# Kernel tuning notes

Hardware: AMD Instinct MI355X
Metric: run time of the kernel (lower is better)

## Reference

```python
import jax, jax.numpy as jnp
import numpy as np

E, TOPK, H, I = 8, 2, 2048, 5632
T = 4096


def setup_inputs() -> dict:
    key = jax.random.key(0)
    k1, k2, k3, k4 = jax.random.split(key, 4)
    hidden_states = jax.random.normal(k1, (T, H), dtype=jnp.float32)
    gate_w = jax.random.normal(k2, (E, H), dtype=jnp.float32) * (1.0 / np.sqrt(H))
    # fused gate+up projection: [E, 2*I, H]
    w13 = jax.random.normal(k3, (E, 2 * I, H), dtype=jnp.float32) * (1.0 / np.sqrt(H))
    # down projection: [E, H, I]
    w2 = jax.random.normal(k4, (E, H, I), dtype=jnp.float32) * (1.0 / np.sqrt(I))
    return {"hidden_states": hidden_states, "gate_w": gate_w, "w13": w13, "w2": w2, "top_k": TOPK}


def reference(hidden_states, gate_w, w13, w2, top_k):
    num_experts = gate_w.shape[0]
    inter = w2.shape[2]
    # router: fp32 gate logits -> softmax -> top-k -> renormalize (FusedMoE renormalize=True)
    logits = hidden_states.astype(jnp.float32) @ gate_w.T          # [T, E]
    probs = jax.nn.softmax(logits, axis=-1)
    vals, idx = jax.lax.top_k(probs, top_k)                        # [T, k]
    vals = vals / jnp.sum(vals, axis=-1, keepdims=True)
    # dense routing weight matrix [T, E] (zero outside top-k)
    dense_w = jnp.sum(jax.nn.one_hot(idx, num_experts, dtype=vals.dtype) * vals[..., None], axis=1)

    def body(acc, inputs):
        w13_e, w2_e, we = inputs                                   # [2I,H], [H,I], [T]
        gu = hidden_states @ w13_e.T                               # [T, 2I]
        g, u = gu[:, :inter], gu[:, inter:]
        h = jax.nn.silu(g) * u                                     # SwiGLU
        y = h @ w2_e.T                                             # [T, H]
        return acc + we[:, None] * y, None

    acc0 = jnp.zeros_like(hidden_states)
    out, _ = jax.lax.scan(body, acc0, (w13, w2, dense_w.T))
    return out
```

## Files before the change

### kernel.cpp

```cpp
#include <hip/hip_runtime.h>

#define T_TOK 4096
#define H_DIM 2048
#define I_DIM 5632
#define NE 8

typedef _Float16 f16;
typedef _Float16 f16x8 __attribute__((ext_vector_type(8)));
typedef _Float16 f16x4 __attribute__((ext_vector_type(4)));
typedef float f32x4 __attribute__((ext_vector_type(4)));

#define OFF_META   0
#define OFF_BTOK   256
#define OFF_BW     (256 + 32768)
#define OFF_RE     (256 + 2 * 32768)
#define OFF_RW     (256 + 3 * 32768)
#define OFF_HSB    (256 + 4 * 32768)
#define OFF_HB     (OFF_HSB + (size_t)T_TOK * H_DIM * 2)

__device__ __forceinline__ int swzk(int r, int bir) {
    return (bir & 15) | ((((bir >> 4) ^ r) & 7) << 4);
}

__device__ __forceinline__ f16x4 cvt4(float4 v) {
    f16x4 t; t[0] = (f16)v.x; t[1] = (f16)v.y; t[2] = (f16)v.z; t[3] = (f16)v.w; return t;
}

__global__ void cvt_hs_kernel(const float* __restrict__ hs, f16* __restrict__ hsb) {
    size_t i = ((size_t)blockIdx.x * 256 + threadIdx.x) * 8;
    float4 a = *(const float4*)(hs + i);
    float4 b = *(const float4*)(hs + i + 4);
    f16x8 v;
    v[0] = (f16)a.x; v[1] = (f16)a.y; v[2] = (f16)a.z; v[3] = (f16)a.w;
    v[4] = (f16)b.x; v[5] = (f16)b.y; v[6] = (f16)b.z; v[7] = (f16)b.w;
    *(f16x8*)(hsb + i) = v;
}

__global__ void gate_kernel(const float* __restrict__ hs, const float* __restrict__ gw,
                            int* __restrict__ re, float* __restrict__ rw,
                            int* __restrict__ counts) {
    int lane = threadIdx.x & 63;
    int t = blockIdx.x * 4 + (threadIdx.x >> 6);
    float acc[NE];
#pragma unroll
    for (int e = 0; e < NE; ++e) acc[e] = 0.f;
    const float* x = hs + (size_t)t * H_DIM;
    for (int i = lane; i < H_DIM; i += 64) {
        float xv = x[i];
#pragma unroll
        for (int e = 0; e < NE; ++e) acc[e] += xv * gw[e * H_DIM + i];
    }
#pragma unroll
    for (int e = 0; e < NE; ++e)
        for (int off = 32; off > 0; off >>= 1) acc[e] += __shfl_xor(acc[e], off);
    if (lane == 0) {
        int i1 = 0; float l1 = acc[0];
#pragma unroll
        for (int e = 1; e < NE; ++e) if (acc[e] > l1) { l1 = acc[e]; i1 = e; }
        int i2 = -1; float l2 = -1e30f;
#pragma unroll
        for (int e = 0; e < NE; ++e) if (e != i1 && acc[e] > l2) { l2 = acc[e]; i2 = e; }
        float aa = __expf(l2 - l1);
        float s = 1.f / (1.f + aa);
        re[t * 2] = i1; re[t * 2 + 1] = i2;
        rw[t * 2] = s;  rw[t * 2 + 1] = aa * s;
        atomicAdd(&counts[i1], 1);
        atomicAdd(&counts[i2], 1);
    }
}

__global__ void scan_kernel(int* __restrict__ meta) {
    if (threadIdx.x == 0) {
        int s = 0;
        for (int e = 0; e < NE; ++e) { meta[8 + e] = s; meta[16 + e] = s; s += meta[e]; }
    }
}

__global__ void place_kernel(const int* __restrict__ re, const float* __restrict__ rw,
                             int* __restrict__ cursor, int* __restrict__ btok,
                             float* __restrict__ bwv) {
    int t = blockIdx.x * 256 + threadIdx.x;
    if (t >= T_TOK) return;
#pragma unroll
    for (int s = 0; s < 2; ++s) {
        int e = re[t * 2 + s];
        int p = atomicAdd(&cursor[e], 1);
        btok[p] = t;
        bwv[p] = rw[t * 2 + s];
    }
}

__device__ __forceinline__ void decode_panel(int id, int npx, int e_arg,
                                             int& e, int& bx, int& by) {
    int sg  = id >> 8;
    int rem = id & 255;
    by = rem >> 3;
    int P = sg * 8 + (rem & 7);
    if (e_arg >= 0) { e = e_arg; bx = P; }
    else            { e = P / npx; bx = P % npx; }
}

__global__ __launch_bounds__(512) void gemm1_kernel(
    const float* __restrict__ w13, const f16* __restrict__ hsb, f16* __restrict__ hb,
    const int* __restrict__ counts, const int* __restrict__ offs,
    const int* __restrict__ btok, int e_arg, int global_h)
{
    int e, bx, by;
    decode_panel(blockIdx.x, 88, e_arg, e, bx, by);
    const int n_e = counts[e];
    if (by * 128 >= n_e) return;
    const int boff = offs[e];
    const float* We = w13 + (size_t)e * (2 * I_DIM) * H_DIM;

    const int tid = threadIdx.x;
    const int lane = tid & 63;
    const int wid = tid >> 6;
    const int wm = wid >> 1, wn = wid & 1;

    __shared__ f16 As[128 * 64];
    __shared__ f16 Bg[64 * 64];
    __shared__ f16 Bu[64 * 64];
    char* AsB = (char*)As; char* BgB = (char*)Bg; char* BuB = (char*)Bu;

    const f16* gA[2];
    int awadr[2];
#pragma unroll
    for (int i = 0; i < 2; ++i) {
        int c = i * 512 + tid;
        int r = c >> 3;
        int s = c & 7;
        int idx = by * 128 + r;
        idx = idx < n_e ? idx : n_e - 1;
        int tok = btok[boff + idx];
        gA[i] = hsb + (size_t)tok * H_DIM + s * 8;
        awadr[i] = r * 128 + swzk(r, s * 16);
    }
    const float* gBg[2]; const float* gBu[2];
    int bwadr[2];
#pragma unroll
    for (int j = 0; j < 2; ++j) {
        int c = j * 512 + tid;
        int r = c >> 4;
        int k4 = c & 15;
        gBg[j] = We + (size_t)(bx * 64 + r) * H_DIM + k4 * 4;
        gBu[j] = We + (size_t)(I_DIM + bx * 64 + r) * H_DIM + k4 * 4;
        bwadr[j] = r * 128 + swzk(r, k4 * 8);
    }

    f32x4 accg[2][2], accu[2][2];
#pragma unroll
    for (int m = 0; m < 2; ++m)
#pragma unroll
        for (int n = 0; n < 2; ++n) { accg[m][n] = (f32x4)0.f; accu[m][n] = (f32x4)0.f; }

    const int NT = H_DIM / 64;

    f16x8 aR[2]; float4 gR[2], uR[2];
#pragma unroll
    for (int i = 0; i < 2; ++i) {
        aR[i] = *(const f16x8*)(gA[i]);
        gR[i] = *(const float4*)(gBg[i]);
        uR[i] = *(const float4*)(gBu[i]);
    }

#pragma unroll 1
    for (int kt = 0; kt < NT; ++kt) {
        __syncthreads();
#pragma unroll
        for (int i = 0; i < 2; ++i) {
            *(f16x8*)(AsB + awadr[i]) = aR[i];
            *(f16x4*)(BgB + bwadr[i]) = cvt4(gR[i]);
            *(f16x4*)(BuB + bwadr[i]) = cvt4(uR[i]);
        }
        __syncthreads();
        if (kt + 1 < NT) {
            int k0 = (kt + 1) * 64;
#pragma unroll
            for (int i = 0; i < 2; ++i) {
                aR[i] = *(const f16x8*)(gA[i] + k0);
                gR[i] = *(const float4*)(gBg[i] + k0);
                uR[i] = *(const float4*)(gBu[i] + k0);
            }
        }
#pragma unroll
        for (int kh = 0; kh < 2; ++kh) {
            f16x8 a[2], bg[2], bu[2];
            const int kb = kh * 64 + (lane >> 4) * 16;
#pragma unroll
            for (int m = 0; m < 2; ++m) {
                int r = wm * 32 + m * 16 + (lane & 15);
                a[m] = *(const f16x8*)(AsB + r * 128 + swzk(r, kb));
            }
#pragma unroll
            for (int n = 0; n < 2; ++n) {
                int r = wn * 32 + n * 16 + (lane & 15);
                bg[n] = *(const f16x8*)(BgB + r * 128 + swzk(r, kb));
                bu[n] = *(const f16x8*)(BuB + r * 128 + swzk(r, kb));
            }
#pragma unroll
            for (int m = 0; m < 2; ++m)
#pragma unroll
                for (int n = 0; n < 2; ++n) {
                    accg[m][n] = __builtin_amdgcn_mfma_f32_16x16x32_f16(a[m], bg[n], accg[m][n], 0, 0, 0);
                    accu[m][n] = __builtin_amdgcn_mfma_f32_16x16x32_f16(a[m], bu[n], accu[m][n], 0, 0, 0);
                }
        }
    }

    const int hbase = (global_h ? boff : 0) + by * 128;
#pragma unroll
    for (int m = 0; m < 2; ++m) {
        int rl0 = wm * 32 + m * 16 + ((lane >> 4) << 2);
#pragma unroll
        for (int r = 0; r < 4; ++r) {
            int rl = rl0 + r;
            if (by * 128 + rl < n_e) {
#pragma unroll
                for (int n = 0; n < 2; ++n) {
                    float g = accg[m][n][r];
                    float u = accu[m][n][r];
                    float h = g / (1.f + __expf(-g)) * u;
                    hb[(size_t)(hbase + rl) * I_DIM + bx * 64 + wn * 32 + n * 16 + (lane & 15)] = (f16)h;
                }
            }
        }
    }
}

__global__ __launch_bounds__(512) void gemm2_kernel(
    const float* __restrict__ w2, const f16* __restrict__ hb, float* __restrict__ out,
    const int* __restrict__ counts, const int* __restrict__ offs,
    const int* __restrict__ btok, const float* __restrict__ bwv, int e_arg, int global_h)
{
    int e, bx, by;
    decode_panel(blockIdx.x, 16, e_arg, e, bx, by);
    const int n_e = counts[e];
    if (by * 128 >= n_e) return;
    const int boff = offs[e];
    const float* We = w2 + (size_t)e * H_DIM * I_DIM;

    const int tid = threadIdx.x;
    const int lane = tid & 63;
    const int wid = tid >> 6;
    const int wm = wid >> 1, wn = wid & 1;

    __shared__ f16 As[128 * 64];
    __shared__ f16 Bs[128 * 64];
    char* AsB = (char*)As; char* BsB = (char*)Bs;

    const int hbase = (global_h ? boff : 0) + by * 128;
    const f16* gA[2];
    int awadr[2];
#pragma unroll
    for (int i = 0; i < 2; ++i) {
        int c = i * 512 + tid;
        int r = c >> 3;
        int s = c & 7;
        gA[i] = hb + (size_t)(hbase + r) * I_DIM + s * 8;
        awadr[i] = r * 128 + swzk(r, s * 16);
    }
    const float* gB[4];
    int bwadr[4];
#pragma unroll
    for (int j = 0; j < 4; ++j) {
        int c = j * 512 + tid;
        int r = c >> 4;
        int k4 = c & 15;
        gB[j] = We + (size_t)(bx * 128 + r) * I_DIM + k4 * 4;
        bwadr[j] = r * 128 + swzk(r, k4 * 8);
    }

    f32x4 acc[2][4];
#pragma unroll
    for (int m = 0; m < 2; ++m)
#pragma unroll
        for (int n = 0; n < 4; ++n) acc[m][n] = (f32x4)0.f;

    const int NT = I_DIM / 64;

    f16x8 aR[2]; float4 bR[4];
#pragma unroll
    for (int i = 0; i < 2; ++i) aR[i] = *(const f16x8*)(gA[i]);
#pragma unroll
    for (int j = 0; j < 4; ++j) bR[j] = *(const float4*)(gB[j]);

#pragma unroll 1
    for (int kt = 0; kt < NT; ++kt) {
        __syncthreads();
#pragma unroll
        for (int i = 0; i < 2; ++i) *(f16x8*)(AsB + awadr[i]) = aR[i];
#pragma unroll
        for (int j = 0; j < 4; ++j) *(f16x4*)(BsB + bwadr[j]) = cvt4(bR[j]);
        __syncthreads();
        if (kt + 1 < NT) {
            int k0 = (kt + 1) * 64;
#pragma unroll
            for (int i = 0; i < 2; ++i) aR[i] = *(const f16x8*)(gA[i] + k0);
#pragma unroll
            for (int j = 0; j < 4; ++j) bR[j] = *(const float4*)(gB[j] + k0);
        }
#pragma unroll
        for (int kh = 0; kh < 2; ++kh) {
            f16x8 a[2], b[4];
            const int kb = kh * 64 + (lane >> 4) * 16;
#pragma unroll
            for (int m = 0; m < 2; ++m) {
                int r = wm * 32 + m * 16 + (lane & 15);
                a[m] = *(const f16x8*)(AsB + r * 128 + swzk(r, kb));
            }
#pragma unroll
            for (int n = 0; n < 4; ++n) {
                int r = wn * 64 + n * 16 + (lane & 15);
                b[n] = *(const f16x8*)(BsB + r * 128 + swzk(r, kb));
            }
#pragma unroll
            for (int m = 0; m < 2; ++m)
#pragma unroll
                for (int n = 0; n < 4; ++n)
                    acc[m][n] = __builtin_amdgcn_mfma_f32_16x16x32_f16(a[m], b[n], acc[m][n], 0, 0, 0);
        }
    }

#pragma unroll
    for (int m = 0; m < 2; ++m) {
        int rl0 = wm * 32 + m * 16 + ((lane >> 4) << 2);
#pragma unroll
        for (int r = 0; r < 4; ++r) {
            int rl = rl0 + r;
            if (by * 128 + rl < n_e) {
                int p = boff + by * 128 + rl;
                int tok = btok[p];
                float w = bwv[p];
#pragma unroll
                for (int n = 0; n < 4; ++n)
                    atomicAdd(&out[(size_t)tok * H_DIM + bx * 128 + wn * 64 + n * 16 + (lane & 15)],
                              w * acc[m][n][r]);
            }
        }
    }
}

extern "C" void kernel_launch(void* const* d_in, const int* in_sizes, int n_in,
                              void* d_out, int out_size, void* d_ws, size_t ws_size,
                              hipStream_t stream) {
    const float* hs  = (const float*)d_in[0];
    const float* gw  = (const float*)d_in[1];
    const float* w13 = (const float*)d_in[2];
    const float* w2  = (const float*)d_in[3];
    float* out = (float*)d_out;

    char* ws = (char*)d_ws;
    int*   meta = (int*)(ws + OFF_META);
    int*   btok = (int*)(ws + OFF_BTOK);
    float* bwv  = (float*)(ws + OFF_BW);
    int*   re   = (int*)(ws + OFF_RE);
    float* rw   = (float*)(ws + OFF_RW);
    f16*   hsb  = (f16*)(ws + OFF_HSB);
    f16*   hb   = (f16*)(ws + OFF_HB);

    hipMemsetAsync(d_out, 0, (size_t)T_TOK * H_DIM * 4, stream);
    hipMemsetAsync(meta, 0, 256, stream);

    cvt_hs_kernel<<<(T_TOK * H_DIM) / (256 * 8), 256, 0, stream>>>(hs, hsb);
    gate_kernel<<<T_TOK / 4, 256, 0, stream>>>(hs, gw, re, rw, meta);
    scan_kernel<<<1, 64, 0, stream>>>(meta);
    place_kernel<<<T_TOK / 256, 256, 0, stream>>>(re, rw, meta + 16, btok, bwv);

    size_t need_allpairs = OFF_HB + (size_t)(2 * T_TOK + 128) * I_DIM * 2;
    if (ws_size >= need_allpairs) {
        gemm1_kernel<<<704 * 32, 512, 0, stream>>>(w13, hsb, hb, meta, meta + 8, btok, -1, 1);
        gemm2_kernel<<<128 * 32, 512, 0, stream>>>(w2, hb, out, meta, meta + 8, btok, bwv, -1, 1);
    } else {
        for (int e = 0; e < NE; ++e) {
            gemm1_kernel<<<88 * 32, 512, 0, stream>>>(w13, hsb, hb, meta, meta + 8, btok, e, 0);
            gemm2_kernel<<<16 * 32, 512, 0, stream>>>(w2, hb, out, meta, meta + 8, btok, bwv, e, 0);
        }
    }
}
```

Baseline: 1.152 ms.

## Double-buffer shared memory tiles in both MoE GEMM kernels

Both GEMM kernels switch from a single shared-memory tile with two barriers per K step to ping-pong buffers with one barrier per step. Global loads for the next tile are issued before the MFMA work on the current buffer and written to the other buffer afterward. This overlaps LDS stores and global latency with compute and halves barrier count. LDS usage doubles (up to 64 KB for gemm2), which may lower occupancy.

New measurement: 1.330 ms. 1.15x slower.

```diff
diff --git a/kernel.cpp b/kernel.cpp
--- a/kernel.cpp
+++ b/kernel.cpp
@@ -117,10 +117,9 @@
     const int wid = tid >> 6;
     const int wm = wid >> 1, wn = wid & 1;
 
-    __shared__ f16 As[128 * 64];
-    __shared__ f16 Bg[64 * 64];
-    __shared__ f16 Bu[64 * 64];
-    char* AsB = (char*)As; char* BgB = (char*)Bg; char* BuB = (char*)Bu;
+    __shared__ f16 As0[128 * 64], As1[128 * 64];
+    __shared__ f16 Bg0[64 * 64],  Bg1[64 * 64];
+    __shared__ f16 Bu0[64 * 64],  Bu1[64 * 64];
 
     const f16* gA[2];
     int awadr[2];
@@ -155,57 +154,72 @@
 
     const int NT = H_DIM / 64;
 
-    f16x8 aR[2]; float4 gR[2], uR[2];
-#pragma unroll
-    for (int i = 0; i < 2; ++i) {
-        aR[i] = *(const f16x8*)(gA[i]);
-        gR[i] = *(const float4*)(gBg[i]);
-        uR[i] = *(const float4*)(gBu[i]);
-    }
-
-#pragma unroll 1
-    for (int kt = 0; kt < NT; ++kt) {
-        __syncthreads();
-#pragma unroll
-        for (int i = 0; i < 2; ++i) {
-            *(f16x8*)(AsB + awadr[i]) = aR[i];
-            *(f16x4*)(BgB + bwadr[i]) = cvt4(gR[i]);
-            *(f16x4*)(BuB + bwadr[i]) = cvt4(uR[i]);
+    {
+        f16x8 aP[2]; float4 gP[2], uP[2];
+#pragma unroll
+        for (int i = 0; i < 2; ++i) aP[i] = *(const f16x8*)(gA[i]);
+#pragma unroll
+        for (int j = 0; j < 2; ++j) { gP[j] = *(const float4*)gBg[j]; uP[j] = *(const float4*)gBu[j]; }
+#pragma unroll
+        for (int i = 0; i < 2; ++i) *(f16x8*)((char*)As0 + awadr[i]) = aP[i];
+#pragma unroll
+        for (int j = 0; j < 2; ++j) {
+            *(f16x4*)((char*)Bg0 + bwadr[j]) = cvt4(gP[j]);
+            *(f16x4*)((char*)Bu0 + bwadr[j]) = cvt4(uP[j]);
         }
         __syncthreads();
-        if (kt + 1 < NT) {
-            int k0 = (kt + 1) * 64;
-#pragma unroll
-            for (int i = 0; i < 2; ++i) {
-                aR[i] = *(const f16x8*)(gA[i] + k0);
-                gR[i] = *(const float4*)(gBg[i] + k0);
-                uR[i] = *(const float4*)(gBu[i] + k0);
-            }
-        }
-#pragma unroll
-        for (int kh = 0; kh < 2; ++kh) {
-            f16x8 a[2], bg[2], bu[2];
-            const int kb = kh * 64 + (lane >> 4) * 16;
-#pragma unroll
-            for (int m = 0; m < 2; ++m) {
-                int r = wm * 32 + m * 16 + (lane & 15);
-                a[m] = *(const f16x8*)(AsB + r * 128 + swzk(r, kb));
-            }
-#pragma unroll
-            for (int n = 0; n < 2; ++n) {
-                int r = wn * 32 + n * 16 + (lane & 15);
-                bg[n] = *(const f16x8*)(BgB + r * 128 + swzk(r, kb));
-                bu[n] = *(const f16x8*)(BuB + r * 128 + swzk(r, kb));
-            }
-#pragma unroll
-            for (int m = 0; m < 2; ++m)
-#pragma unroll
-                for (int n = 0; n < 2; ++n) {
-                    accg[m][n] = __builtin_amdgcn_mfma_f32_16x16x32_f16(a[m], bg[n], accg[m][n], 0, 0, 0);
-                    accu[m][n] = __builtin_amdgcn_mfma_f32_16x16x32_f16(a[m], bu[n], accu[m][n], 0, 0, 0);
-                }
-        }
-    }
+    }
+
+#define G1_TILE(AsR, BgR, BuR, AsW, BgW, BuW, t)                                    \
+    {                                                                               \
+        const int kn = (((t) + 1 < NT) ? (t) + 1 : NT - 1) * 64;                    \
+        f16x8 aN[2]; float4 gN[2], uN[2];                                           \
+        _Pragma("unroll")                                                           \
+        for (int i = 0; i < 2; ++i) aN[i] = *(const f16x8*)(gA[i] + kn);            \
+        _Pragma("unroll")                                                           \
+        for (int j = 0; j < 2; ++j) {                                               \
+            gN[j] = *(const float4*)(gBg[j] + kn);                                  \
+            uN[j] = *(const float4*)(gBu[j] + kn);                                  \
+        }                                                                           \
+        _Pragma("unroll")                                                           \
+        for (int kh = 0; kh < 2; ++kh) {                                            \
+            f16x8 a[2], bg[2], bu[2];                                               \
+            const int kb = kh * 64 + (lane >> 4) * 16;                              \
+            _Pragma("unroll")                                                       \
+            for (int m = 0; m < 2; ++m) {                                           \
+                int r = wm * 32 + m * 16 + (lane & 15);                             \
+                a[m] = *(const f16x8*)((const char*)AsR + r * 128 + swzk(r, kb));   \
+            }                                                                       \
+            _Pragma("unroll")                                                       \
+            for (int n = 0; n < 2; ++n) {                                           \
+                int r = wn * 32 + n * 16 + (lane & 15);                             \
+                bg[n] = *(const f16x8*)((const char*)BgR + r * 128 + swzk(r, kb));  \
+                bu[n] = *(const f16x8*)((const char*)BuR + r * 128 + swzk(r, kb));  \
+            }                                                                       \
+            _Pragma("unroll")                                                       \
+            for (int m = 0; m < 2; ++m)                                             \
+                _Pragma("unroll")                                                   \
+                for (int n = 0; n < 2; ++n) {                                       \
+                    accg[m][n] = __builtin_amdgcn_mfma_f32_16x16x32_f16(a[m], bg[n], accg[m][n], 0, 0, 0); \
+                    accu[m][n] = __builtin_amdgcn_mfma_f32_16x16x32_f16(a[m], bu[n], accu[m][n], 0, 0, 0); \
+                }                                                                   \
+        }                                                                           \
+        _Pragma("unroll")                                                           \
+        for (int i = 0; i < 2; ++i) *(f16x8*)((char*)AsW + awadr[i]) = aN[i];       \
+        _Pragma("unroll")                                                           \
+        for (int j = 0; j < 2; ++j) {                                               \
+            *(f16x4*)((char*)BgW + bwadr[j]) = cvt4(gN[j]);                         \
+            *(f16x4*)((char*)BuW + bwadr[j]) = cvt4(uN[j]);                         \
+        }                                                                           \
+        __syncthreads();                                                            \
+    }
+
+#pragma unroll 1
+    for (int kt = 0; kt < NT; kt += 2) {
+        G1_TILE(As0, Bg0, Bu0, As1, Bg1, Bu1, kt);
+        G1_TILE(As1, Bg1, Bu1, As0, Bg0, Bu0, kt + 1);
+    }
+#undef G1_TILE
 
     const int hbase = (global_h ? boff : 0) + by * 128;
 #pragma unroll
@@ -244,9 +258,8 @@
     const int wid = tid >> 6;
     const int wm = wid >> 1, wn = wid & 1;
 
-    __shared__ f16 As[128 * 64];
-    __shared__ f16 Bs[128 * 64];
-    char* AsB = (char*)As; char* BsB = (char*)Bs;
+    __shared__ f16 As0[128 * 64], As1[128 * 64];
+    __shared__ f16 Bs0[128 * 64], Bs1[128 * 64];
 
     const int hbase = (global_h ? boff : 0) + by * 128;
     const f16* gA[2];
@@ -278,48 +291,60 @@
 
     const int NT = I_DIM / 64;
 
-    f16x8 aR[2]; float4 bR[4];
-#pragma unroll
-    for (int i = 0; i < 2; ++i) aR[i] = *(const f16x8*)(gA[i]);
-#pragma unroll
-    for (int j = 0; j < 4; ++j) bR[j] = *(const float4*)(gB[j]);
+    {
+        f16x8 aP[2]; float4 bP[4];
+#pragma unroll
+        for (int i = 0; i < 2; ++i) aP[i] = *(const f16x8*)(gA[i]);
+#pragma unroll
+        for (int j = 0; j < 4; ++j) bP[j] = *(const float4*)gB[j];
+#pragma unroll
+        for (int i = 0; i < 2; ++i) *(f16x8*)((char*)As0 + awadr[i]) = aP[i];
+#pragma unroll
+        for (int j = 0; j < 4; ++j) *(f16x4*)((char*)Bs0 + bwadr[j]) = cvt4(bP[j]);
+        __syncthreads();
+    }
+
+#define G2_TILE(AsR, BsR, AsW, BsW, t)                                              \
+    {                                                                               \
+        const int kn = (((t) + 1 < NT) ? (t) + 1 : NT - 1) * 64;                    \
+        f16x8 aN[2]; float4 bN[4];                                                  \
+        _Pragma("unroll")                                                           \
+        for (int i = 0; i < 2; ++i) aN[i] = *(const f16x8*)(gA[i] + kn);            \
+        _Pragma("unroll")                                                           \
+        for (int j = 0; j < 4; ++j) bN[j] = *(const float4*)(gB[j] + kn);           \
+        _Pragma("unroll")                                                           \
+        for (int kh = 0; kh < 2; ++kh) {                                            \
+            f16x8 a[2], b[4];                                                       \
+            const int kb = kh * 64 + (lane >> 4) * 16;                              \
+            _Pragma("unroll")                                                       \
+            for (int m = 0; m < 2; ++m) {                                           \
+                int r = wm * 32 + m * 16 + (lane & 15);                             \
+                a[m] = *(const f16x8*)((const char*)AsR + r * 128 + swzk(r, kb));   \
+            }                                                                       \
+            _Pragma("unroll")                                                       \
+            for (int n = 0; n < 4; ++n) {                                           \
+                int r = wn * 64 + n * 16 + (lane & 15);                             \
+                b[n] = *(const f16x8*)((const char*)BsR + r * 128 + swzk(r, kb));   \
+            }                                                                       \
+            _Pragma("unroll")                                                       \
+            for (int m = 0; m < 2; ++m)                                             \
+                _Pragma("unroll")                                                   \
+                for (int n = 0; n < 4; ++n)                                         \
+                    acc[m][n] = __builtin_amdgcn_mfma_f32_16x16x32_f16(a[m], b[n], acc[m][n], 0, 0, 0); \
+        }                                                                           \
+        _Pragma("unroll")                                                           \
+        for (int i = 0; i < 2; ++i) *(f16x8*)((char*)AsW + awadr[i]) = aN[i];       \
+        _Pragma("unroll")                                                           \
+        for (int j = 0; j < 4; ++j) *(f16x4*)((char*)BsW + bwadr[j]) = cvt4(bN[j]); \
+        __syncthreads();                                                            \
+    }
 
 #pragma unroll 1
-    for (int kt = 0; kt < NT; ++kt) {
-        __syncthreads();
-#pragma unroll
-        for (int i = 0; i < 2; ++i) *(f16x8*)(AsB + awadr[i]) = aR[i];
-#pragma unroll
-        for (int j = 0; j < 4; ++j) *(f16x4*)(BsB + bwadr[j]) = cvt4(bR[j]);
-        __syncthreads();
-        if (kt + 1 < NT) {
-            int k0 = (kt + 1) * 64;
-#pragma unroll
-            for (int i = 0; i < 2; ++i) aR[i] = *(const f16x8*)(gA[i] + k0);
-#pragma unroll
-            for (int j = 0; j < 4; ++j) bR[j] = *(const float4*)(gB[j] + k0);
-        }
-#pragma unroll
-        for (int kh = 0; kh < 2; ++kh) {
-            f16x8 a[2], b[4];
-            const int kb = kh * 64 + (lane >> 4) * 16;
-#pragma unroll
-            for (int m = 0; m < 2; ++m) {
-                int r = wm * 32 + m * 16 + (lane & 15);
-                a[m] = *(const f16x8*)(AsB + r * 128 + swzk(r, kb));
-            }
-#pragma unroll
-            for (int n = 0; n < 4; ++n) {
-                int r = wn * 64 + n * 16 + (lane & 15);
-                b[n] = *(const f16x8*)(BsB + r * 128 + swzk(r, kb));
-            }
-#pragma unroll
-            for (int m = 0; m < 2; ++m)
-#pragma unroll
-                for (int n = 0; n < 4; ++n)
-                    acc[m][n] = __builtin_amdgcn_mfma_f32_16x16x32_f16(a[m], b[n], acc[m][n], 0, 0, 0);
-        }
-    }
+    for (int kt = 0; kt < NT; kt += 2) {
+        G2_TILE(As0, Bs0, As1, Bs1, kt);
+        G2_TILE(As1, Bs1, As0, Bs0, kt + 1);
+    }
+#undef G2_TILE
 
 #pragma unroll
     for (int m = 0; m < 2; ++m) {
```

## Double-buffer MoE GEMMs with direct global-to-LDS loads and larger tiles

Applied to the files above, without the earlier changes.

Both expert GEMM kernels move to 128x256 tiles with 8 waves arranged 2x4. LDS is double-buffered, and activations load straight into LDS through global_load_lds using a pre-swizzled source. The fp32 weight loads are split into two halves that are converted and staged while MFMAs run, with raw waitcnt/barrier control and setprio around the MFMA bursts. Launch grids shrink to match. The aim is to hide global latency and raise MFMA reuse per loaded byte, at the cost of more LDS and registers (launch_bounds 512,2) and fragile hand-managed waitcnts.

Result: slower. 1.648 ms (+43.1%).

```diff
diff --git a/kernel.cpp b/kernel.cpp
--- a/kernel.cpp
+++ b/kernel.cpp
@@ -18,12 +18,23 @@
 #define OFF_HSB    (256 + 4 * 32768)
 #define OFF_HB     (OFF_HSB + (size_t)T_TOK * H_DIM * 2)
 
+typedef const __attribute__((address_space(1))) unsigned int guint;
+typedef __attribute__((address_space(3))) unsigned int luint;
+
+#define WAITVM8()   asm volatile("s_waitcnt vmcnt(8)" ::: "memory")
+#define WAITVM0()   asm volatile("s_waitcnt vmcnt(0)" ::: "memory")
+#define LGKM0_SB()  do { asm volatile("s_waitcnt lgkmcnt(0)" ::: "memory"); __builtin_amdgcn_sched_barrier(0); } while (0)
+
 __device__ __forceinline__ int swzk(int r, int bir) {
     return (bir & 15) | ((((bir >> 4) ^ r) & 7) << 4);
 }
 
 __device__ __forceinline__ f16x4 cvt4(float4 v) {
     f16x4 t; t[0] = (f16)v.x; t[1] = (f16)v.y; t[2] = (f16)v.z; t[3] = (f16)v.w; return t;
+}
+
+__device__ __forceinline__ f16x8 ldsr(const char* base, int r, int kb) {
+    return *(const f16x8*)(base + r * 128 + swzk(r, kb));
 }
 
 __global__ void cvt_hs_kernel(const float* __restrict__ hs, f16* __restrict__ hsb) {
@@ -92,238 +103,326 @@
 
 __device__ __forceinline__ void decode_panel(int id, int npx, int e_arg,
                                              int& e, int& bx, int& by) {
+    if (e_arg >= 0) { e = e_arg; bx = id >> 5; by = id & 31; return; }
     int sg  = id >> 8;
     int rem = id & 255;
     by = rem >> 3;
     int P = sg * 8 + (rem & 7);
-    if (e_arg >= 0) { e = e_arg; bx = P; }
-    else            { e = P / npx; bx = P % npx; }
-}
-
-__global__ __launch_bounds__(512) void gemm1_kernel(
+    e = P / npx; bx = P % npx;
+}
+
+__global__ __launch_bounds__(512, 2) void gemm1_kernel(
     const float* __restrict__ w13, const f16* __restrict__ hsb, f16* __restrict__ hb,
     const int* __restrict__ counts, const int* __restrict__ offs,
     const int* __restrict__ btok, int e_arg, int global_h)
 {
     int e, bx, by;
-    decode_panel(blockIdx.x, 88, e_arg, e, bx, by);
+    decode_panel(blockIdx.x, 44, e_arg, e, bx, by);
     const int n_e = counts[e];
     if (by * 128 >= n_e) return;
     const int boff = offs[e];
     const float* We = w13 + (size_t)e * (2 * I_DIM) * H_DIM;
 
-    const int tid = threadIdx.x;
+    const int tid  = threadIdx.x;
     const int lane = tid & 63;
-    const int wid = tid >> 6;
-    const int wm = wid >> 1, wn = wid & 1;
-
-    __shared__ f16 As[128 * 64];
-    __shared__ f16 Bg[64 * 64];
-    __shared__ f16 Bu[64 * 64];
-    char* AsB = (char*)As; char* BgB = (char*)Bg; char* BuB = (char*)Bu;
+    const int wid  = tid >> 6;
+    const int wm   = wid >> 2;
+    const int wn   = wid & 3;
+    const int l15  = lane & 15;
+    const int klo  = (lane >> 4) * 16;
+
+    __shared__ f16 As[2][128 * 64];
+    __shared__ f16 Bs[2][256 * 64];
+    char* AsB = (char*)As; char* BsB = (char*)Bs;
 
     const f16* gA[2];
-    int awadr[2];
+    int adst[2];
 #pragma unroll
     for (int i = 0; i < 2; ++i) {
         int c = i * 512 + tid;
         int r = c >> 3;
-        int s = c & 7;
         int idx = by * 128 + r;
         idx = idx < n_e ? idx : n_e - 1;
         int tok = btok[boff + idx];
-        gA[i] = hsb + (size_t)tok * H_DIM + s * 8;
-        awadr[i] = r * 128 + swzk(r, s * 16);
-    }
-    const float* gBg[2]; const float* gBu[2];
-    int bwadr[2];
-#pragma unroll
-    for (int j = 0; j < 2; ++j) {
+        gA[i] = hsb + (size_t)tok * H_DIM + ((c & 7) ^ (r & 7)) * 8;
+        adst[i] = c * 16;
+    }
+    const float* gB[8];
+    int bwadr[8];
+#pragma unroll
+    for (int j = 0; j < 8; ++j) {
         int c = j * 512 + tid;
-        int r = c >> 4;
+        int row = c >> 4;
         int k4 = c & 15;
-        gBg[j] = We + (size_t)(bx * 64 + r) * H_DIM + k4 * 4;
-        gBu[j] = We + (size_t)(I_DIM + bx * 64 + r) * H_DIM + k4 * 4;
-        bwadr[j] = r * 128 + swzk(r, k4 * 8);
-    }
-
-    f32x4 accg[2][2], accu[2][2];
-#pragma unroll
-    for (int m = 0; m < 2; ++m)
-#pragma unroll
-        for (int n = 0; n < 2; ++n) { accg[m][n] = (f32x4)0.f; accu[m][n] = (f32x4)0.f; }
+        int wrow = (row < 128) ? (bx * 128 + row) : (I_DIM + bx * 128 + (row - 128));
+        gB[j] = We + (size_t)wrow * H_DIM + k4 * 4;
+        bwadr[j] = row * 128 + swzk(row, k4 * 8);
+    }
+
+    f32x4 ag[4][2], au[4][2];
+#pragma unroll
+    for (int m = 0; m < 4; ++m)
+#pragma unroll
+        for (int n = 0; n < 2; ++n) { ag[m][n] = (f32x4)0.f; au[m][n] = (f32x4)0.f; }
 
     const int NT = H_DIM / 64;
 
-    f16x8 aR[2]; float4 gR[2], uR[2];
-#pragma unroll
-    for (int i = 0; i < 2; ++i) {
-        aR[i] = *(const f16x8*)(gA[i]);
-        gR[i] = *(const float4*)(gBg[i]);
-        uR[i] = *(const float4*)(gBu[i]);
-    }
+    float4 bX[4], bY[4];
+#pragma unroll
+    for (int i = 0; i < 2; ++i)
+        __builtin_amdgcn_global_load_lds((guint*)gA[i], (luint*)(AsB + adst[i]), 16, 0, 0);
+#pragma unroll
+    for (int j = 0; j < 4; ++j) bX[j] = *(const float4*)gB[j];
+#pragma unroll
+    for (int j = 0; j < 4; ++j) bY[j] = *(const float4*)gB[j + 4];
+#pragma unroll
+    for (int j = 0; j < 4; ++j) *(f16x4*)(BsB + bwadr[j])     = cvt4(bX[j]);
+#pragma unroll
+    for (int j = 0; j < 4; ++j) *(f16x4*)(BsB + bwadr[j + 4]) = cvt4(bY[j]);
+#pragma unroll
+    for (int j = 0; j < 4; ++j) bX[j] = *(const float4*)(gB[j] + 64);
+#pragma unroll
+    for (int j = 0; j < 4; ++j) bY[j] = *(const float4*)(gB[j + 4] + 64);
+    asm volatile("s_waitcnt lgkmcnt(0)" ::: "memory");
+    __builtin_amdgcn_s_barrier();
 
 #pragma unroll 1
     for (int kt = 0; kt < NT; ++kt) {
-        __syncthreads();
-#pragma unroll
-        for (int i = 0; i < 2; ++i) {
-            *(f16x8*)(AsB + awadr[i]) = aR[i];
-            *(f16x4*)(BgB + bwadr[i]) = cvt4(gR[i]);
-            *(f16x4*)(BuB + bwadr[i]) = cvt4(uR[i]);
-        }
-        __syncthreads();
-        if (kt + 1 < NT) {
-            int k0 = (kt + 1) * 64;
-#pragma unroll
-            for (int i = 0; i < 2; ++i) {
-                aR[i] = *(const f16x8*)(gA[i] + k0);
-                gR[i] = *(const float4*)(gBg[i] + k0);
-                uR[i] = *(const float4*)(gBu[i] + k0);
-            }
-        }
-#pragma unroll
-        for (int kh = 0; kh < 2; ++kh) {
-            f16x8 a[2], bg[2], bu[2];
-            const int kb = kh * 64 + (lane >> 4) * 16;
-#pragma unroll
-            for (int m = 0; m < 2; ++m) {
-                int r = wm * 32 + m * 16 + (lane & 15);
-                a[m] = *(const f16x8*)(AsB + r * 128 + swzk(r, kb));
-            }
-#pragma unroll
-            for (int n = 0; n < 2; ++n) {
-                int r = wn * 32 + n * 16 + (lane & 15);
-                bg[n] = *(const f16x8*)(BgB + r * 128 + swzk(r, kb));
-                bu[n] = *(const f16x8*)(BuB + r * 128 + swzk(r, kb));
-            }
-#pragma unroll
-            for (int m = 0; m < 2; ++m)
-#pragma unroll
-                for (int n = 0; n < 2; ++n) {
-                    accg[m][n] = __builtin_amdgcn_mfma_f32_16x16x32_f16(a[m], bg[n], accg[m][n], 0, 0, 0);
-                    accu[m][n] = __builtin_amdgcn_mfma_f32_16x16x32_f16(a[m], bu[n], accu[m][n], 0, 0, 0);
-                }
-        }
-    }
+        const int cur = kt & 1;
+        const int kA = ((kt + 1 < NT) ? kt + 1 : NT - 1) * 64;
+        const int kB = ((kt + 2 < NT) ? kt + 2 : NT - 1) * 64;
+        const char* Ab = AsB + cur * 16384;
+        const char* Bb = BsB + cur * 32768;
+        char* Aw = AsB + (cur ^ 1) * 16384;
+        char* Bw = BsB + (cur ^ 1) * 32768;
+        {
+#pragma unroll
+            for (int i = 0; i < 2; ++i)
+                __builtin_amdgcn_global_load_lds((guint*)(gA[i] + kA), (luint*)(Aw + adst[i]), 16, 0, 0);
+            f16x8 af[2][4], bf[2][2];
+#pragma unroll
+            for (int kh = 0; kh < 2; ++kh) {
+                const int kb = kh * 64 + klo;
+#pragma unroll
+                for (int mf = 0; mf < 4; ++mf) af[kh][mf] = ldsr(Ab, wm * 64 + mf * 16 + l15, kb);
+#pragma unroll
+                for (int nf = 0; nf < 2; ++nf) bf[kh][nf] = ldsr(Bb, wn * 32 + nf * 16 + l15, kb);
+            }
+#pragma unroll
+            for (int j = 0; j < 4; ++j) *(f16x4*)(Bw + bwadr[j]) = cvt4(bX[j]);
+            __builtin_amdgcn_s_barrier();
+            LGKM0_SB();
+            __builtin_amdgcn_s_setprio(1);
+#pragma unroll
+            for (int kh = 0; kh < 2; ++kh)
+#pragma unroll
+                for (int mf = 0; mf < 4; ++mf)
+#pragma unroll
+                    for (int nf = 0; nf < 2; ++nf)
+                        ag[mf][nf] = __builtin_amdgcn_mfma_f32_16x16x32_f16(af[kh][mf], bf[kh][nf], ag[mf][nf], 0, 0, 0);
+            __builtin_amdgcn_s_setprio(0);
+            __builtin_amdgcn_s_barrier();
+        }
+        {
+#pragma unroll
+            for (int j = 0; j < 4; ++j) bX[j] = *(const float4*)(gB[j] + kB);
+            f16x8 af[2][4], bf[2][2];
+#pragma unroll
+            for (int kh = 0; kh < 2; ++kh) {
+                const int kb = kh * 64 + klo;
+#pragma unroll
+                for (int mf = 0; mf < 4; ++mf) af[kh][mf] = ldsr(Ab, wm * 64 + mf * 16 + l15, kb);
+#pragma unroll
+                for (int nf = 0; nf < 2; ++nf) bf[kh][nf] = ldsr(Bb, 128 + wn * 32 + nf * 16 + l15, kb);
+            }
+#pragma unroll
+            for (int j = 0; j < 4; ++j) *(f16x4*)(Bw + bwadr[j + 4]) = cvt4(bY[j]);
+#pragma unroll
+            for (int j = 0; j < 4; ++j) bY[j] = *(const float4*)(gB[j + 4] + kB);
+            __builtin_amdgcn_s_barrier();
+            LGKM0_SB();
+            __builtin_amdgcn_s_setprio(1);
+#pragma unroll
+            for (int kh = 0; kh < 2; ++kh)
+#pragma unroll
+                for (int mf = 0; mf < 4; ++mf)
+#pragma unroll
+                    for (int nf = 0; nf < 2; ++nf)
+                        au[mf][nf] = __builtin_amdgcn_mfma_f32_16x16x32_f16(af[kh][mf], bf[kh][nf], au[mf][nf], 0, 0, 0);
+            __builtin_amdgcn_s_setprio(0);
+            WAITVM8();
+            __builtin_amdgcn_s_barrier();
+        }
+    }
+    WAITVM0();
 
     const int hbase = (global_h ? boff : 0) + by * 128;
 #pragma unroll
-    for (int m = 0; m < 2; ++m) {
-        int rl0 = wm * 32 + m * 16 + ((lane >> 4) << 2);
+    for (int mf = 0; mf < 4; ++mf) {
+        int rl0 = wm * 64 + mf * 16 + ((lane >> 4) << 2);
 #pragma unroll
         for (int r = 0; r < 4; ++r) {
             int rl = rl0 + r;
             if (by * 128 + rl < n_e) {
 #pragma unroll
-                for (int n = 0; n < 2; ++n) {
-                    float g = accg[m][n][r];
-                    float u = accu[m][n][r];
+                for (int nf = 0; nf < 2; ++nf) {
+                    float g = ag[mf][nf][r];
+                    float u = au[mf][nf][r];
                     float h = g / (1.f + __expf(-g)) * u;
-                    hb[(size_t)(hbase + rl) * I_DIM + bx * 64 + wn * 32 + n * 16 + (lane & 15)] = (f16)h;
+                    hb[(size_t)(hbase + rl) * I_DIM + bx * 128 + wn * 32 + nf * 16 + l15] = (f16)h;
                 }
             }
         }
     }
 }
 
-__global__ __launch_bounds__(512) void gemm2_kernel(
+__global__ __launch_bounds__(512, 2) void gemm2_kernel(
     const float* __restrict__ w2, const f16* __restrict__ hb, float* __restrict__ out,
     const int* __restrict__ counts, const int* __restrict__ offs,
     const int* __restrict__ btok, const float* __restrict__ bwv, int e_arg, int global_h)
 {
     int e, bx, by;
-    decode_panel(blockIdx.x, 16, e_arg, e, bx, by);
+    decode_panel(blockIdx.x, 8, e_arg, e, bx, by);
     const int n_e = counts[e];
     if (by * 128 >= n_e) return;
     const int boff = offs[e];
     const float* We = w2 + (size_t)e * H_DIM * I_DIM;
 
-    const int tid = threadIdx.x;
+    const int tid  = threadIdx.x;
     const int lane = tid & 63;
-    const int wid = tid >> 6;
-    const int wm = wid >> 1, wn = wid & 1;
-
-    __shared__ f16 As[128 * 64];
-    __shared__ f16 Bs[128 * 64];
+    const int wid  = tid >> 6;
+    const int wm   = wid >> 2;
+    const int wn   = wid & 3;
+    const int l15  = lane & 15;
+    const int klo  = (lane >> 4) * 16;
+
+    __shared__ f16 As[2][128 * 64];
+    __shared__ f16 Bs[2][256 * 64];
     char* AsB = (char*)As; char* BsB = (char*)Bs;
 
-    const int hbase = (global_h ? boff : 0) + by * 128;
+    const int hb0 = global_h ? boff : 0;
     const f16* gA[2];
-    int awadr[2];
+    int adst[2];
 #pragma unroll
     for (int i = 0; i < 2; ++i) {
         int c = i * 512 + tid;
         int r = c >> 3;
-        int s = c & 7;
-        gA[i] = hb + (size_t)(hbase + r) * I_DIM + s * 8;
-        awadr[i] = r * 128 + swzk(r, s * 16);
-    }
-    const float* gB[4];
-    int bwadr[4];
-#pragma unroll
-    for (int j = 0; j < 4; ++j) {
+        int idx = by * 128 + r;
+        idx = idx < n_e ? idx : n_e - 1;
+        gA[i] = hb + (size_t)(hb0 + idx) * I_DIM + ((c & 7) ^ (r & 7)) * 8;
+        adst[i] = c * 16;
+    }
+    const float* gB[8];
+    int bwadr[8];
+#pragma unroll
+    for (int j = 0; j < 8; ++j) {
         int c = j * 512 + tid;
-        int r = c >> 4;
+        int row = c >> 4;
         int k4 = c & 15;
-        gB[j] = We + (size_t)(bx * 128 + r) * I_DIM + k4 * 4;
-        bwadr[j] = r * 128 + swzk(r, k4 * 8);
-    }
-
-    f32x4 acc[2][4];
-#pragma unroll
-    for (int m = 0; m < 2; ++m)
+        gB[j] = We + (size_t)(bx * 256 + row) * I_DIM + k4 * 4;
+        bwadr[j] = row * 128 + swzk(row, k4 * 8);
+    }
+
+    f32x4 acc[4][4];
+#pragma unroll
+    for (int m = 0; m < 4; ++m)
 #pragma unroll
         for (int n = 0; n < 4; ++n) acc[m][n] = (f32x4)0.f;
 
     const int NT = I_DIM / 64;
 
-    f16x8 aR[2]; float4 bR[4];
-#pragma unroll
-    for (int i = 0; i < 2; ++i) aR[i] = *(const f16x8*)(gA[i]);
-#pragma unroll
-    for (int j = 0; j < 4; ++j) bR[j] = *(const float4*)(gB[j]);
+    float4 bX[4], bY[4];
+#pragma unroll
+    for (int i = 0; i < 2; ++i)
+        __builtin_amdgcn_global_load_lds((guint*)gA[i], (luint*)(AsB + adst[i]), 16, 0, 0);
+#pragma unroll
+    for (int j = 0; j < 4; ++j) bX[j] = *(const float4*)gB[j];
+#pragma unroll
+    for (int j = 0; j < 4; ++j) bY[j] = *(const float4*)gB[j + 4];
+#pragma unroll
+    for (int j = 0; j < 4; ++j) *(f16x4*)(BsB + bwadr[j])     = cvt4(bX[j]);
+#pragma unroll
+    for (int j = 0; j < 4; ++j) *(f16x4*)(BsB + bwadr[j + 4]) = cvt4(bY[j]);
+#pragma unroll
+    for (int j = 0; j < 4; ++j) bX[j] = *(const float4*)(gB[j] + 64);
+#pragma unroll
+    for (int j = 0; j < 4; ++j) bY[j] = *(const float4*)(gB[j + 4] + 64);
+    asm volatile("s_waitcnt lgkmcnt(0)" ::: "memory");
+    __builtin_amdgcn_s_barrier();
 
 #pragma unroll 1
     for (int kt = 0; kt < NT; ++kt) {
-        __syncthreads();
-#pragma unroll
-        for (int i = 0; i < 2; ++i) *(f16x8*)(AsB + awadr[i]) = aR[i];
-#pragma unroll
-        for (int j = 0; j < 4; ++j) *(f16x4*)(BsB + bwadr[j]) = cvt4(bR[j]);
-        __syncthreads();
-        if (kt + 1 < NT) {
-            int k0 = (kt + 1) * 64;
-#pragma unroll
-            for (int i = 0; i < 2; ++i) aR[i] = *(const f16x8*)(gA[i] + k0);
-#pragma unroll
-            for (int j = 0; j < 4; ++j) bR[j] = *(const float4*)(gB[j] + k0);
-        }
-#pragma unroll
-        for (int kh = 0; kh < 2; ++kh) {
-            f16x8 a[2], b[4];
-            const int kb = kh * 64 + (lane >> 4) * 16;
-#pragma unroll
-            for (int m = 0; m < 2; ++m) {
-                int r = wm * 32 + m * 16 + (lane & 15);
-                a[m] = *(const f16x8*)(AsB + r * 128 + swzk(r, kb));
-            }
-#pragma unroll
-            for (int n = 0; n < 4; ++n) {
-                int r = wn * 64 + n * 16 + (lane & 15);
-                b[n] = *(const f16x8*)(BsB + r * 128 + swzk(r, kb));
-            }
-#pragma unroll
-            for (int m = 0; m < 2; ++m)
-#pragma unroll
-                for (int n = 0; n < 4; ++n)
-                    acc[m][n] = __builtin_amdgcn_mfma_f32_16x16x32_f16(a[m], b[n], acc[m][n], 0, 0, 0);
-        }
-    }
-
-#pragma unroll
-    for (int m = 0; m < 2; ++m) {
-        int rl0 = wm * 32 + m * 16 + ((lane >> 4) << 2);
+        const int cur = kt & 1;
+        const int kA = ((kt + 1 < NT) ? kt + 1 : NT - 1) * 64;
+        const int kB = ((kt + 2 < NT) ? kt + 2 : NT - 1) * 64;
+        const char* Ab = AsB + cur * 16384;
+        const char* Bb = BsB + cur * 32768;
+        char* Aw = AsB + (cur ^ 1) * 16384;
+        char* Bw = BsB + (cur ^ 1) * 32768;
+        {
+#pragma unroll
+            for (int i = 0; i < 2; ++i)
+                __builtin_amdgcn_global_load_lds((guint*)(gA[i] + kA), (luint*)(Aw + adst[i]), 16, 0, 0);
+            f16x8 af[2][4], bf[2][2];
+#pragma unroll
+            for (int kh = 0; kh < 2; ++kh) {
+                const int kb = kh * 64 + klo;
+#pragma unroll
+                for (int mf = 0; mf < 4; ++mf) af[kh][mf] = ldsr(Ab, wm * 64 + mf * 16 + l15, kb);
+#pragma unroll
+                for (int nf = 0; nf < 2; ++nf) bf[kh][nf] = ldsr(Bb, wn * 64 + nf * 16 + l15, kb);
+            }
+#pragma unroll
+            for (int j = 0; j < 4; ++j) *(f16x4*)(Bw + bwadr[j]) = cvt4(bX[j]);
+            __builtin_amdgcn_s_barrier();
+            LGKM0_SB();
+            __builtin_amdgcn_s_setprio(1);
+#pragma unroll
+            for (int kh = 0; kh < 2; ++kh)
+#pragma unroll
+                for (int mf = 0; mf < 4; ++mf)
+#pragma unroll
+                    for (int nf = 0; nf < 2; ++nf)
+                        acc[mf][nf] = __builtin_amdgcn_mfma_f32_16x16x32_f16(af[kh][mf], bf[kh][nf], acc[mf][nf], 0, 0, 0);
+            __builtin_amdgcn_s_setprio(0);
+            __builtin_amdgcn_s_barrier();
+        }
+        {
+#pragma unroll
+            for (int j = 0; j < 4; ++j) bX[j] = *(const float4*)(gB[j] + kB);
+            f16x8 af[2][4], bf[2][2];
+#pragma unroll
+            for (int kh = 0; kh < 2; ++kh) {
+                const int kb = kh * 64 + klo;
+#pragma unroll
+                for (int mf = 0; mf < 4; ++mf) af[kh][mf] = ldsr(Ab, wm * 64 + mf * 16 + l15, kb);
+#pragma unroll
+                for (int nf = 0; nf < 2; ++nf) bf[kh][nf] = ldsr(Bb, wn * 64 + (nf + 2) * 16 + l15, kb);
+            }
+#pragma unroll
+            for (int j = 0; j < 4; ++j) *(f16x4*)(Bw + bwadr[j + 4]) = cvt4(bY[j]);
+#pragma unroll
+            for (int j = 0; j < 4; ++j) bY[j] = *(const float4*)(gB[j + 4] + kB);
+            __builtin_amdgcn_s_barrier();
+            LGKM0_SB();
+            __builtin_amdgcn_s_setprio(1);
+#pragma unroll
+            for (int kh = 0; kh < 2; ++kh)
+#pragma unroll
+                for (int mf = 0; mf < 4; ++mf)
+#pragma unroll
+                    for (int nf = 0; nf < 2; ++nf)
+                        acc[mf][nf + 2] = __builtin_amdgcn_mfma_f32_16x16x32_f16(af[kh][mf], bf[kh][nf], acc[mf][nf + 2], 0, 0, 0);
+            __builtin_amdgcn_s_setprio(0);
+            WAITVM8();
+            __builtin_amdgcn_s_barrier();
+        }
+    }
+    WAITVM0();
+
+#pragma unroll
+    for (int mf = 0; mf < 4; ++mf) {
+        int rl0 = wm * 64 + mf * 16 + ((lane >> 4) << 2);
 #pragma unroll
         for (int r = 0; r < 4; ++r) {
             int rl = rl0 + r;
@@ -332,9 +431,9 @@
                 int tok = btok[p];
                 float w = bwv[p];
 #pragma unroll
-                for (int n = 0; n < 4; ++n)
-                    atomicAdd(&out[(size_t)tok * H_DIM + bx * 128 + wn * 64 + n * 16 + (lane & 15)],
-                              w * acc[m][n][r]);
+                for (int nf = 0; nf < 4; ++nf)
+                    atomicAdd(&out[(size_t)tok * H_DIM + bx * 256 + wn * 64 + nf * 16 + l15],
+                              w * acc[mf][nf][r]);
             }
         }
     }
@@ -368,12 +467,12 @@
 
     size_t need_allpairs = OFF_HB + (size_t)(2 * T_TOK + 128) * I_DIM * 2;
     if (ws_size >= need_allpairs) {
-        gemm1_kernel<<<704 * 32, 512, 0, stream>>>(w13, hsb, hb, meta, meta + 8, btok, -1, 1);
-        gemm2_kernel<<<128 * 32, 512, 0, stream>>>(w2, hb, out, meta, meta + 8, btok, bwv, -1, 1);
+        gemm1_kernel<<<352 * 32, 512, 0, stream>>>(w13, hsb, hb, meta, meta + 8, btok, -1, 1);
+        gemm2_kernel<<<64 * 32, 512, 0, stream>>>(w2, hb, out, meta, meta + 8, btok, bwv, -1, 1);
     } else {
         for (int e = 0; e < NE; ++e) {
-            gemm1_kernel<<<88 * 32, 512, 0, stream>>>(w13, hsb, hb, meta, meta + 8, btok, e, 0);
-            gemm2_kernel<<<16 * 32, 512, 0, stream>>>(w2, hb, out, meta, meta + 8, btok, bwv, e, 0);
-        }
-    }
-}
+            gemm1_kernel<<<44 * 32, 512, 0, stream>>>(w13, hsb, hb, meta, meta + 8, btok, e, 0);
+            gemm2_kernel<<<8 * 32, 512, 0, stream>>>(w2, hb, out, meta, meta + 8, btok, bwv, e, 0);
+        }
+    }
+}
```
